# Kernel optimization log

Hardware: AMD Instinct MI355X
Metric: run time of the kernel (lower is better)

Reference implementation:

```python
import jax, jax.numpy as jnp
import numpy as np

N_NODES = 100000
N_EDGES = 1600000
N_GRAPHS = 256
IN_F = 64   # global_features (GNN input dim)
OUT_F = 64  # node_features (GNN output dim)


def setup_inputs() -> dict:
    key = jax.random.key(0)
    ks = jax.random.split(key, 8)
    x = jax.random.normal(ks[0], (N_NODES, IN_F), dtype=jnp.float32)
    edge_index = jax.random.randint(ks[1], (2, N_EDGES), 0, N_NODES, dtype=jnp.int64)
    batch = jnp.sort(jax.random.randint(ks[2], (N_NODES,), 0, N_GRAPHS, dtype=jnp.int64))
    # GNNLayer linear: in=global_features, out=node_features
    W_gnn = jax.random.normal(ks[3], (IN_F, OUT_F), dtype=jnp.float32) / np.sqrt(IN_F)
    b_gnn = jnp.zeros((OUT_F,), dtype=jnp.float32)
    # global_attention: Linear(node_features, 1)
    W_att = jax.random.normal(ks[4], (OUT_F, 1), dtype=jnp.float32) / np.sqrt(OUT_F)
    b_att = jnp.zeros((1,), dtype=jnp.float32)
    return {"x": x, "edge_index": edge_index, "batch": batch,
            "W_gnn": W_gnn, "b_gnn": b_gnn, "W_att": W_att, "b_att": b_att}


def reference(x, edge_index, batch, W_gnn, b_gnn, W_att, b_att):
    src, dst = edge_index[0], edge_index[1]
    # --- GNN message passing layer: aggregate neighbor features, transform ---
    agg = jax.ops.segment_sum(x[src], dst, num_segments=N_NODES)  # [N, IN_F]
    h = jax.nn.relu((x + agg) @ W_gnn + b_gnn)                    # [N, OUT_F]
    # --- attention scores + scatter softmax over batch segments ---
    scores = (h @ W_att + b_att)[:, 0]                            # [N]
    seg_max = jax.ops.segment_max(scores, batch, num_segments=N_GRAPHS)
    e = jnp.exp(scores - seg_max[batch])
    denom = jax.ops.segment_sum(e, batch, num_segments=N_GRAPHS)
    w = e / denom[batch]                                          # [N]
    # --- weighted scatter-add pooling ---
    out = jax.ops.segment_sum(w[:, None] * h, batch, num_segments=N_GRAPHS)
    return out  # [N_GRAPHS, OUT_F]
```

## Files before the change

### kernel.cpp

```cpp
#include <hip/hip_runtime.h>

#define N_NODES  100000
#define N_EDGES  1600000
#define N_GRAPHS 256
#define F        64

#define BSHIFT   8
#define BNODES   256
#define NBUCKET  391
#define CHUNK    8192
#define NCHUNK   196

__global__ __launch_bounds__(1024) void hist_kernel(
        const int* __restrict__ dst, int* __restrict__ cnt) {
    __shared__ int hist[NBUCKET];
    int tid = threadIdx.x;
    for (int b = tid; b < NBUCKET; b += 1024) hist[b] = 0;
    __syncthreads();
    int base = blockIdx.x * CHUNK;
    int end  = min(base + CHUNK, N_EDGES);
    for (int e = base + tid; e < end; e += 1024)
        atomicAdd(&hist[dst[e] >> BSHIFT], 1);
    __syncthreads();
    for (int b = tid; b < NBUCKET; b += 1024)
        cnt[blockIdx.x * NBUCKET + b] = hist[b];
}

__global__ __launch_bounds__(512) void chunk_scan_kernel(
        const int* __restrict__ cnt, int* __restrict__ start, int* __restrict__ bbase) {
    __shared__ int t[512];
    int b = threadIdx.x;
    int tot = 0;
    if (b < NBUCKET)
        for (int c = 0; c < NCHUNK; ++c) tot += cnt[c * NBUCKET + b];
    t[b] = (b < NBUCKET) ? tot : 0;
    __syncthreads();
    #pragma unroll
    for (int o = 1; o < 512; o <<= 1) {
        int u = (b >= o) ? t[b - o] : 0;
        __syncthreads();
        t[b] += u;
        __syncthreads();
    }
    if (b < NBUCKET) {
        int base = t[b] - tot;
        bbase[b] = base;
        if (b == NBUCKET - 1) bbase[NBUCKET] = t[b];
        int run = base;
        for (int c = 0; c < NCHUNK; ++c) {
            start[c * NBUCKET + b] = run;
            run += cnt[c * NBUCKET + b];
        }
    }
}

__global__ __launch_bounds__(1024) void scatter_kernel(
        const int* __restrict__ src, const int* __restrict__ dst,
        const int* __restrict__ start, unsigned int* __restrict__ pairs) {
    __shared__ int cur[NBUCKET];
    int tid = threadIdx.x;
    for (int b = tid; b < NBUCKET; b += 1024)
        cur[b] = start[blockIdx.x * NBUCKET + b];
    __syncthreads();
    int base = blockIdx.x * CHUNK;
    int end  = min(base + CHUNK, N_EDGES);
    for (int e = base + tid; e < end; e += 1024) {
        int d = dst[e];
        int slot = atomicAdd(&cur[d >> BSHIFT], 1);
        pairs[slot] = ((unsigned)(d & (BNODES - 1)) << 17) | (unsigned)src[e];
    }
}

__global__ __launch_bounds__(1024) void bucket_sort_kernel(
        const unsigned int* __restrict__ pairs,
        const int* __restrict__ bbase,
        int* __restrict__ eidx, int* __restrict__ noff) {
    __shared__ int cnt[BNODES];
    __shared__ int pref[BNODES];
    __shared__ int cur[BNODES];
    int tid = threadIdx.x;
    int b = blockIdx.x;
    int lo = bbase[b], hi = bbase[b + 1];

    if (tid < BNODES) cnt[tid] = 0;
    __syncthreads();
    for (int e = lo + tid; e < hi; e += 1024)
        atomicAdd(&cnt[pairs[e] >> 17], 1);
    __syncthreads();
    if (tid < BNODES) pref[tid] = cnt[tid];
    __syncthreads();
    #pragma unroll
    for (int o = 1; o < BNODES; o <<= 1) {
        int u = (tid < BNODES && tid >= o) ? pref[tid - o] : 0;
        __syncthreads();
        if (tid < BNODES) pref[tid] += u;
        __syncthreads();
    }
    if (tid < BNODES) {
        int excl = lo + pref[tid] - cnt[tid];
        cur[tid] = excl;
        int node = b * BNODES + tid;
        if (node < N_NODES) noff[node] = excl;
        if (node == N_NODES - 1) noff[N_NODES] = hi;
    }
    __syncthreads();
    for (int e = lo + tid; e < hi; e += 1024) {
        unsigned int p = pairs[e];
        int slot = atomicAdd(&cur[p >> 17], 1);
        eidx[slot] = (int)(p & 0x1FFFFu);
    }
}

#define GT_BLOCKS 1024
#define GT_WAVES  (GT_BLOCKS * 4)

__global__ __launch_bounds__(256, 4) void gather_transform_kernel(
        const float* __restrict__ x,
        const int*   __restrict__ noff,
        const int*   __restrict__ eidx,
        const float* __restrict__ Wg,
        const float* __restrict__ bg,
        const float* __restrict__ Wa,
        const float* __restrict__ ba,
        float*       __restrict__ h,
        float*       __restrict__ scores) {
    int tid  = threadIdx.x;
    int lane = tid & 63;
    int grp  = lane >> 4;
    int c    = lane & 15;
    int waveId = blockIdx.x * 4 + (tid >> 6);

    float wcol[F];
    #pragma unroll
    for (int k = 0; k < F; ++k) wcol[k] = Wg[k * F + lane];
    float bgl = bg[lane];
    float wal = Wa[lane];
    float ba0 = ba[0];

    const float4* x4 = (const float4*)x;

    for (int n = waveId; n < N_NODES; n += GT_WAVES) {
        int start = noff[n];
        int end   = noff[n + 1];

        float4 a = make_float4(0.f, 0.f, 0.f, 0.f);
        for (int base = start; base < end; base += 64) {
            int jmax = end - base; if (jmax > 64) jmax = 64;
            int sl = (base + lane < end) ? eidx[base + lane] : 0;
            for (int j = 0; j < jmax; j += 4) {
                int el = j + grp;
                int s  = __shfl(sl, el, 64);
                if (el < jmax) {
                    float4 v = x4[s * 16 + c];
                    a.x += v.x; a.y += v.y; a.z += v.z; a.w += v.w;
                }
            }
        }
        #pragma unroll
        for (int o = 16; o <= 32; o <<= 1) {
            a.x += __shfl_xor(a.x, o, 64);
            a.y += __shfl_xor(a.y, o, 64);
            a.z += __shfl_xor(a.z, o, 64);
            a.w += __shfl_xor(a.w, o, 64);
        }
        { float4 v = x4[n * 16 + c]; a.x += v.x; a.y += v.y; a.z += v.z; a.w += v.w; }

        float re[4] = {a.x, a.y, a.z, a.w};
        float acc0 = 0.f, acc1 = 0.f, acc2 = 0.f, acc3 = 0.f;
        #pragma unroll
        for (int k = 0; k < F; k += 4) {
            float r0 = __int_as_float(__builtin_amdgcn_readlane(__float_as_int(re[0]), k >> 2));
            float r1 = __int_as_float(__builtin_amdgcn_readlane(__float_as_int(re[1]), k >> 2));
            float r2 = __int_as_float(__builtin_amdgcn_readlane(__float_as_int(re[2]), k >> 2));
            float r3 = __int_as_float(__builtin_amdgcn_readlane(__float_as_int(re[3]), k >> 2));
            acc0 += r0 * wcol[k + 0];
            acc1 += r1 * wcol[k + 1];
            acc2 += r2 * wcol[k + 2];
            acc3 += r3 * wcol[k + 3];
        }
        float hv = (acc0 + acc1) + (acc2 + acc3) + bgl;
        hv = hv > 0.f ? hv : 0.f;
        h[n * F + lane] = hv;

        float p = hv * wal;
        #pragma unroll
        for (int o = 32; o > 0; o >>= 1)
            p += __shfl_down(p, o, 64);
        if (lane == 0) scores[n] = p + ba0;
    }
}

__device__ __forceinline__ int lower_bound_i(const int* __restrict__ a, int n, int key) {
    int lo = 0, hi = n;
    while (lo < hi) {
        int mid = (lo + hi) >> 1;
        if (a[mid] < key) lo = mid + 1; else hi = mid;
    }
    return lo;
}

#define POOL_THREADS 512
#define POOL_WAVES   (POOL_THREADS / 64)

__global__ __launch_bounds__(POOL_THREADS) void attn_pool_kernel(
        const float* __restrict__ h,
        const float* __restrict__ scores,
        const int*   __restrict__ batch,
        float*       __restrict__ out) {
    int g = blockIdx.x;
    int tid  = threadIdx.x;
    int wave = tid >> 6;
    int lane = tid & 63;
    int grp  = lane >> 4;
    int c    = lane & 15;

    int lo = lower_bound_i(batch, N_NODES, g);
    int hi = lower_bound_i(batch, N_NODES, g + 1);

    __shared__ float red[POOL_THREADS];
    float m = -INFINITY;
    for (int n = lo + tid; n < hi; n += POOL_THREADS) m = fmaxf(m, scores[n]);
    red[tid] = m;
    __syncthreads();
    #pragma unroll
    for (int s = POOL_THREADS / 2; s > 0; s >>= 1) {
        if (tid < s) red[tid] = fmaxf(red[tid], red[tid + s]);
        __syncthreads();
    }
    m = red[0];
    __syncthreads();

    const float4* h4 = (const float4*)h;
    float4 acc = make_float4(0.f, 0.f, 0.f, 0.f);
    float den = 0.f;
    for (int base = lo + wave * 4; base < hi; base += POOL_WAVES * 4) {
        int n = base + grp;
        if (n < hi) {
            float e = __expf(scores[n] - m);
            den += e;
            float4 v = h4[n * 16 + c];
            acc.x += e * v.x; acc.y += e * v.y; acc.z += e * v.z; acc.w += e * v.w;
        }
    }
    #pragma unroll
    for (int o = 16; o <= 32; o <<= 1) {
        acc.x += __shfl_xor(acc.x, o, 64);
        acc.y += __shfl_xor(acc.y, o, 64);
        acc.z += __shfl_xor(acc.z, o, 64);
        acc.w += __shfl_xor(acc.w, o, 64);
        den   += __shfl_xor(den,   o, 64);
    }

    __shared__ float4 accs4[POOL_WAVES][16];
    __shared__ float  dens[POOL_WAVES];
    if (lane < 16) accs4[wave][c] = acc;
    if (lane == 0) dens[wave] = den;
    __syncthreads();

    if (wave == 0) {
        const float* accsf = (const float*)accs4;
        float a = 0.f, d = 0.f;
        #pragma unroll
        for (int w = 0; w < POOL_WAVES; ++w) { a += accsf[w * F + lane]; d += dens[w]; }
        out[g * F + lane] = (hi > lo) ? a / d : 0.f;
    }
}

extern "C" void kernel_launch(void* const* d_in, const int* in_sizes, int n_in,
                              void* d_out, int out_size, void* d_ws, size_t ws_size,
                              hipStream_t stream) {
    const float* x     = (const float*)d_in[0];
    const int*   ei    = (const int*)d_in[1];
    const int*   batch = (const int*)d_in[2];
    const float* Wg    = (const float*)d_in[3];
    const float* bg    = (const float*)d_in[4];
    const float* Wa    = (const float*)d_in[5];
    const float* ba    = (const float*)d_in[6];
    float* out = (float*)d_out;

    const int* src = ei;
    const int* dst = ei + N_EDGES;

    char* ws = (char*)d_ws;
    int*          cnt    = (int*)(ws);
    int*          start  = (int*)(ws +   306688);
    int*          bbase  = (int*)(ws +   613376);
    unsigned int* pairs  = (unsigned int*)(ws +  615168);
    int*          eidx   = (int*)(ws +  7015168);
    int*          noff   = (int*)(ws + 13415168);
    float*        h      = (float*)(ws + 13815424);
    float*        scores = (float*)(ws + 39415424);

    hist_kernel        <<<NCHUNK, 1024, 0, stream>>>(dst, cnt);
    chunk_scan_kernel  <<<1, 512, 0, stream>>>(cnt, start, bbase);
    scatter_kernel     <<<NCHUNK, 1024, 0, stream>>>(src, dst, start, pairs);
    bucket_sort_kernel <<<NBUCKET, 1024, 0, stream>>>(pairs, bbase, eidx, noff);
    gather_transform_kernel<<<GT_BLOCKS, 256, 0, stream>>>(
        x, noff, eidx, Wg, bg, Wa, ba, h, scores);
    attn_pool_kernel   <<<N_GRAPHS, POOL_THREADS, 0, stream>>>(h, scores, batch, out);
}
```

Before: 223.9 us.

## Fuse attention softmax pooling into gather-transform kernel with per-graph atomics

The attention-pool kernel is removed and pooling is folded into the gather/transform kernel. Each wave now handles a contiguous run of 25 nodes and accumulates exp(score)·h and exp(score) per graph segment, flushing with atomicAdd whenever the graph id changes. A small finalize kernel then divides by the denominator. This avoids writing and re-reading the full h matrix and the scores array, and drops the separate per-graph max/sum passes. In exchange, the softmax no longer subtracts the segment max, so it relies on scores staying small enough not to overflow exp. It also adds float atomics, so the summation order is nondeterministic.

Result: faster. 218.9 us (-2.2%).

```diff
diff --git a/kernel.cpp b/kernel.cpp
--- a/kernel.cpp
+++ b/kernel.cpp
@@ -111,19 +111,21 @@
     }
 }
 
-#define GT_BLOCKS 1024
-#define GT_WAVES  (GT_BLOCKS * 4)
-
-__global__ __launch_bounds__(256, 4) void gather_transform_kernel(
+#define NODES_PER_WAVE 25
+#define GT_NWAVES  (N_NODES / NODES_PER_WAVE)
+#define GT_BLOCKS  (GT_NWAVES / 4)
+
+__global__ __launch_bounds__(256, 4) void gather_pool_kernel(
         const float* __restrict__ x,
         const int*   __restrict__ noff,
         const int*   __restrict__ eidx,
+        const int*   __restrict__ batch,
         const float* __restrict__ Wg,
         const float* __restrict__ bg,
         const float* __restrict__ Wa,
         const float* __restrict__ ba,
-        float*       __restrict__ h,
-        float*       __restrict__ scores) {
+        float*       __restrict__ out_acc,
+        float*       __restrict__ denom) {
     int tid  = threadIdx.x;
     int lane = tid & 63;
     int grp  = lane >> 4;
@@ -139,7 +141,14 @@
 
     const float4* x4 = (const float4*)x;
 
-    for (int n = waveId; n < N_NODES; n += GT_WAVES) {
+    int n0   = waveId * NODES_PER_WAVE;
+    int nEnd = n0 + NODES_PER_WAVE;
+
+    int   cur_g = batch[n0];
+    float accw  = 0.f;
+    float denw  = 0.f;
+
+    for (int n = n0; n < nEnd; ++n) {
         int start = noff[n];
         int end   = noff[n + 1];
 
@@ -180,90 +189,33 @@
         }
         float hv = (acc0 + acc1) + (acc2 + acc3) + bgl;
         hv = hv > 0.f ? hv : 0.f;
-        h[n * F + lane] = hv;
 
         float p = hv * wal;
         #pragma unroll
         for (int o = 32; o > 0; o >>= 1)
             p += __shfl_down(p, o, 64);
-        if (lane == 0) scores[n] = p + ba0;
-    }
-}
-
-__device__ __forceinline__ int lower_bound_i(const int* __restrict__ a, int n, int key) {
-    int lo = 0, hi = n;
-    while (lo < hi) {
-        int mid = (lo + hi) >> 1;
-        if (a[mid] < key) lo = mid + 1; else hi = mid;
-    }
-    return lo;
-}
-
-#define POOL_THREADS 512
-#define POOL_WAVES   (POOL_THREADS / 64)
-
-__global__ __launch_bounds__(POOL_THREADS) void attn_pool_kernel(
-        const float* __restrict__ h,
-        const float* __restrict__ scores,
-        const int*   __restrict__ batch,
-        float*       __restrict__ out) {
-    int g = blockIdx.x;
-    int tid  = threadIdx.x;
-    int wave = tid >> 6;
-    int lane = tid & 63;
-    int grp  = lane >> 4;
-    int c    = lane & 15;
-
-    int lo = lower_bound_i(batch, N_NODES, g);
-    int hi = lower_bound_i(batch, N_NODES, g + 1);
-
-    __shared__ float red[POOL_THREADS];
-    float m = -INFINITY;
-    for (int n = lo + tid; n < hi; n += POOL_THREADS) m = fmaxf(m, scores[n]);
-    red[tid] = m;
-    __syncthreads();
-    #pragma unroll
-    for (int s = POOL_THREADS / 2; s > 0; s >>= 1) {
-        if (tid < s) red[tid] = fmaxf(red[tid], red[tid + s]);
-        __syncthreads();
-    }
-    m = red[0];
-    __syncthreads();
-
-    const float4* h4 = (const float4*)h;
-    float4 acc = make_float4(0.f, 0.f, 0.f, 0.f);
-    float den = 0.f;
-    for (int base = lo + wave * 4; base < hi; base += POOL_WAVES * 4) {
-        int n = base + grp;
-        if (n < hi) {
-            float e = __expf(scores[n] - m);
-            den += e;
-            float4 v = h4[n * 16 + c];
-            acc.x += e * v.x; acc.y += e * v.y; acc.z += e * v.z; acc.w += e * v.w;
-        }
-    }
-    #pragma unroll
-    for (int o = 16; o <= 32; o <<= 1) {
-        acc.x += __shfl_xor(acc.x, o, 64);
-        acc.y += __shfl_xor(acc.y, o, 64);
-        acc.z += __shfl_xor(acc.z, o, 64);
-        acc.w += __shfl_xor(acc.w, o, 64);
-        den   += __shfl_xor(den,   o, 64);
-    }
-
-    __shared__ float4 accs4[POOL_WAVES][16];
-    __shared__ float  dens[POOL_WAVES];
-    if (lane < 16) accs4[wave][c] = acc;
-    if (lane == 0) dens[wave] = den;
-    __syncthreads();
-
-    if (wave == 0) {
-        const float* accsf = (const float*)accs4;
-        float a = 0.f, d = 0.f;
-        #pragma unroll
-        for (int w = 0; w < POOL_WAVES; ++w) { a += accsf[w * F + lane]; d += dens[w]; }
-        out[g * F + lane] = (hi > lo) ? a / d : 0.f;
-    }
+        float s = __int_as_float(__builtin_amdgcn_readlane(__float_as_int(p), 0)) + ba0;
+        float e = __expf(s);
+
+        int g = batch[n];
+        if (g != cur_g) {
+            atomicAdd(&out_acc[cur_g * F + lane], accw);
+            if (lane == 0) atomicAdd(&denom[cur_g], denw);
+            accw = 0.f; denw = 0.f; cur_g = g;
+        }
+        accw += e * hv;
+        denw += e;
+    }
+    atomicAdd(&out_acc[cur_g * F + lane], accw);
+    if (lane == 0) atomicAdd(&denom[cur_g], denw);
+}
+
+__global__ __launch_bounds__(256) void finalize_kernel(
+        float* __restrict__ out, const float* __restrict__ denom) {
+    int i = blockIdx.x * 256 + threadIdx.x;
+    if (i >= N_GRAPHS * F) return;
+    float d = denom[i >> 6];
+    out[i] = (d > 0.f) ? out[i] / d : 0.f;
 }
 
 extern "C" void kernel_launch(void* const* d_in, const int* in_sizes, int n_in,
@@ -288,14 +240,16 @@
     unsigned int* pairs  = (unsigned int*)(ws +  615168);
     int*          eidx   = (int*)(ws +  7015168);
     int*          noff   = (int*)(ws + 13415168);
-    float*        h      = (float*)(ws + 13815424);
-    float*        scores = (float*)(ws + 39415424);
+    float*        denom  = (float*)(ws + 13815424);
+
+    hipMemsetAsync(out,   0, (size_t)N_GRAPHS * F * sizeof(float), stream);
+    hipMemsetAsync(denom, 0, N_GRAPHS * sizeof(float), stream);
 
     hist_kernel        <<<NCHUNK, 1024, 0, stream>>>(dst, cnt);
     chunk_scan_kernel  <<<1, 512, 0, stream>>>(cnt, start, bbase);
     scatter_kernel     <<<NCHUNK, 1024, 0, stream>>>(src, dst, start, pairs);
     bucket_sort_kernel <<<NBUCKET, 1024, 0, stream>>>(pairs, bbase, eidx, noff);
-    gather_transform_kernel<<<GT_BLOCKS, 256, 0, stream>>>(
-        x, noff, eidx, Wg, bg, Wa, ba, h, scores);
-    attn_pool_kernel   <<<N_GRAPHS, POOL_THREADS, 0, stream>>>(h, scores, batch, out);
-}
+    gather_pool_kernel <<<GT_BLOCKS, 256, 0, stream>>>(
+        x, noff, eidx, batch, Wg, bg, Wa, ba, out, denom);
+    finalize_kernel    <<<(N_GRAPHS * F + 255) / 256, 256, 0, stream>>>(out, denom);
+}
```
